# Kernel tuning notes

Measured on AMD Instinct MI355X. Metric: run time of the kernel, lower is better.

Reference implementation:

```python
import jax, jax.numpy as jnp
import numpy as np
from jax import lax

N_EXPERTS = 8


def setup_inputs() -> dict:
    key = jax.random.key(0)
    ks = jax.random.split(key, 5)
    B, F, H, C, E = 32768, 512, 256, 100, N_EXPERTS
    x = jax.random.normal(ks[0], (B, F), dtype=jnp.float32)
    W1 = jax.random.normal(ks[1], (E, F, H), dtype=jnp.float32) * (1.0 / np.sqrt(F))
    b1 = jnp.zeros((E, H), dtype=jnp.float32)
    W2 = jax.random.normal(ks[2], (E, H, C), dtype=jnp.float32) * (1.0 / np.sqrt(H))
    b2 = jnp.zeros((E, C), dtype=jnp.float32)
    Wg = jax.random.normal(ks[3], (F, E), dtype=jnp.float32) * (1.0 / np.sqrt(F))
    return {"x": x, "W1": W1, "b1": b1, "W2": W2, "b2": b2, "Wg": Wg, "k": 2}


def reference(x, W1, b1, W2, b2, Wg, k):
    B = x.shape[0]
    # experts: per-expert 2-layer MLP, vectorized over the expert dim e
    h = jax.nn.relu(jnp.einsum('bf,efh->ebh', x, W1) + b1[:, None, :])  # [E,B,H]
    preds = jnp.einsum('ebh,ehc->ebc', h, W2) + b2[:, None, :]          # [E,B,C]
    # fixed gating: softmax over gate logits, top-k, hard 1/k weights
    probs = jax.nn.softmax(x @ Wg, axis=-1)                             # [B,E]
    _, top_idx = lax.top_k(probs, k)                                    # [B,k]
    weights = jnp.zeros_like(probs).at[jnp.arange(B)[:, None], top_idx].set(1.0 / k)
    # combined prediction: gate-weighted sum of per-expert softmaxed logits
    combined = jnp.einsum('ebc,be->bc', jax.nn.softmax(preds, axis=-1), weights)
    part_sizes = (weights > 0).sum(axis=0)  # samples routed per expert
    return combined, preds, part_sizes
```

## Files before the change

kernel.cpp:

```cpp
#include <hip/hip_runtime.h>
#include <hip/hip_bf16.h>
#include <math.h>

#define B_ 32768
#define F_ 512
#define H_ 256
#define C_ 100
#define CP 112
#define E_ 8

typedef __attribute__((ext_vector_type(8))) short bf16x8;
typedef __attribute__((ext_vector_type(4))) float f32x4;

__device__ __forceinline__ unsigned short f2b(float f) {
    unsigned int u = __float_as_uint(f);
    return (unsigned short)((u + 0x7fffu + ((u >> 16) & 1u)) >> 16);
}

__device__ __forceinline__ void gll16(const void* g, void* l) {
    __builtin_amdgcn_global_load_lds((__attribute__((address_space(1))) void*)(g),
                                     (__attribute__((address_space(3))) void*)(l),
                                     16, 0, 0);
}

__global__ __launch_bounds__(256) void k0_cvt_x(const float* __restrict__ x,
                                                unsigned short* __restrict__ xb) {
    size_t t = (size_t)blockIdx.x * 256 + threadIdx.x;
    #pragma unroll
    for (int it = 0; it < 4; ++it) {
        size_t i4 = t + (size_t)it * (4096 * 256);
        float4 v = ((const float4*)x)[i4];
        ushort4 o;
        o.x = f2b(v.x); o.y = f2b(v.y); o.z = f2b(v.z); o.w = f2b(v.w);
        ((ushort4*)xb)[i4] = o;
    }
}

__global__ __launch_bounds__(256) void k0_tr_w1(const float* __restrict__ W1,
                                                unsigned short* __restrict__ w1t) {
    __shared__ float tile[32][33];
    int e = blockIdx.z, fb = blockIdx.x * 32, hb = blockIdx.y * 32;
    int tx = threadIdx.x, ty = threadIdx.y;
    #pragma unroll
    for (int j = 0; j < 4; ++j)
        tile[ty + 8 * j][tx] = W1[((size_t)(e * F_ + fb + ty + 8 * j)) * H_ + hb + tx];
    __syncthreads();
    #pragma unroll
    for (int j = 0; j < 4; ++j)
        w1t[((size_t)(e * H_ + hb + ty + 8 * j)) * F_ + fb + tx] = f2b(tile[tx][ty + 8 * j]);
}

__global__ __launch_bounds__(256) void k0_cvt_w2(const float* __restrict__ W2,
                                                 unsigned short* __restrict__ w2t) {
    int idx = blockIdx.x * 256 + threadIdx.x;
    if (idx >= E_ * CP * H_) return;
    int e = idx / (CP * H_);
    int r = idx - e * (CP * H_);
    int c = r / H_, h = r - c * H_;
    float v = (c < C_) ? W2[((size_t)(e * H_ + h)) * C_ + c] : 0.0f;
    w2t[idx] = f2b(v);
}

__global__ __launch_bounds__(256) void k1_gate(const float* __restrict__ x,
                                               const float* __restrict__ Wg,
                                               int* __restrict__ routes,
                                               float* __restrict__ part) {
    __shared__ float sWg[F_ * E_];
    __shared__ int cnt[E_];
    int tid = threadIdx.x;
    for (int i = tid; i < F_ * E_; i += 256) sWg[i] = Wg[i];
    if (tid < E_) cnt[tid] = 0;
    __syncthreads();

    int r = tid >> 3, eidx = tid & 7;
    int row = blockIdx.x * 32 + r;
    const float* xr = x + (size_t)row * F_;
    double acc = 0.0;
    for (int f = 0; f < F_; f += 4) {
        float4 xv = *(const float4*)(xr + f);
        acc += (double)xv.x * (double)sWg[(f + 0) * 8 + eidx];
        acc += (double)xv.y * (double)sWg[(f + 1) * 8 + eidx];
        acc += (double)xv.z * (double)sWg[(f + 2) * 8 + eidx];
        acc += (double)xv.w * (double)sWg[(f + 3) * 8 + eidx];
    }
    double v = acc; int ie = eidx;
    #pragma unroll
    for (int off = 1; off < 8; off <<= 1) {
        double ov = __shfl_xor(v, off);
        int oi = __shfl_xor(ie, off);
        if (ov > v || (ov == v && oi < ie)) { v = ov; ie = oi; }
    }
    int e1 = ie;
    double v2 = (eidx == e1) ? -1e300 : acc; int ie2 = eidx;
    #pragma unroll
    for (int off = 1; off < 8; off <<= 1) {
        double ov = __shfl_xor(v2, off);
        int oi = __shfl_xor(ie2, off);
        if (ov > v2 || (ov == v2 && oi < ie2)) { v2 = ov; ie2 = oi; }
    }
    int e2 = ie2;
    if (eidx == 0) {
        routes[row] = e1 | (e2 << 3);
        atomicAdd(&cnt[e1], 1);
        atomicAdd(&cnt[e2], 1);
    }
    __syncthreads();
    if (tid < E_) atomicAdd(&part[tid], (float)cnt[tid]);
}

__global__ __launch_bounds__(256) void k2_moe(const unsigned short* __restrict__ xbf,
                                              const unsigned short* __restrict__ w1t,
                                              const unsigned short* __restrict__ w2t,
                                              const float* __restrict__ b1,
                                              const float* __restrict__ b2,
                                              float* __restrict__ preds) {
    __shared__ __align__(16) char smem[40960];
    const int tid = threadIdx.x;
    const int w = tid >> 6, lane = tid & 63;
    const int q = lane >> 4, ln = lane & 15;
    const int e = blockIdx.y;
    const int rowBase = blockIdx.x * 64;

    const int sub = lane >> 3;
    const int j8 = (lane & 7) ^ sub;
    const unsigned short* srcA0 = xbf + (size_t)(rowBase + w * 8 + sub) * F_ + 8 * j8;
    const unsigned short* srcB0 = w1t + (size_t)(e * H_ + w * 8 + sub) * F_ + 8 * j8;
    char* dstA = smem + w * 1024;
    char* dstB = smem + 8192 + w * 1024;

    float bias1[4];
    #pragma unroll
    for (int nt = 0; nt < 4; ++nt) bias1[nt] = b1[e * H_ + w * 64 + nt * 16 + ln];

    f32x4 acc[4][4];
    #pragma unroll
    for (int i = 0; i < 4; ++i)
        #pragma unroll
        for (int j = 0; j < 4; ++j) acc[i][j] = (f32x4){0.f, 0.f, 0.f, 0.f};

    for (int kk = 0; kk < 8; ++kk) {
        const int ko = kk * 64;
        gll16(srcA0 + ko, dstA);
        gll16(srcA0 + 32 * F_ + ko, dstA + 4096);
        #pragma unroll
        for (int i = 0; i < 8; ++i)
            gll16(srcB0 + (size_t)i * 32 * F_ + ko, dstB + i * 4096);
        __syncthreads();
        #pragma unroll
        for (int ks = 0; ks < 2; ++ks) {
            const int slot = ((ks * 4 + q) ^ (ln & 7)) * 16;
            bf16x8 af[4], bfr[4];
            #pragma unroll
            for (int mt = 0; mt < 4; ++mt)
                af[mt] = *(const bf16x8*)(smem + (mt * 16 + ln) * 128 + slot);
            #pragma unroll
            for (int nt = 0; nt < 4; ++nt)
                bfr[nt] = *(const bf16x8*)(smem + 8192 + (w * 64 + nt * 16 + ln) * 128 + slot);
            #pragma unroll
            for (int mt = 0; mt < 4; ++mt)
                #pragma unroll
                for (int nt = 0; nt < 4; ++nt)
                    acc[mt][nt] = __builtin_amdgcn_mfma_f32_16x16x32_bf16(af[mt], bfr[nt], acc[mt][nt], 0, 0, 0);
        }
        __syncthreads();
    }

    #pragma unroll
    for (int mt = 0; mt < 4; ++mt)
        #pragma unroll
        for (int nt = 0; nt < 4; ++nt)
            #pragma unroll
            for (int r2 = 0; r2 < 4; ++r2) {
                int rr = mt * 16 + q * 4 + r2;
                int col = w * 64 + nt * 16 + ln;
                float v = fmaxf(acc[mt][nt][r2] + bias1[nt], 0.0f);
                *(unsigned short*)(smem + rr * 528 + col * 2) = f2b(v);
            }

    const unsigned short* w2base = w2t + ((size_t)e * CP + ln) * H_ + q * 8;
    bf16x8 wreg[2][7];
    #pragma unroll
    for (int mt = 0; mt < 7; ++mt)
        wreg[0][mt] = *(const bf16x8*)(w2base + mt * 16 * H_);

    f32x4 acc2[7];
    #pragma unroll
    for (int i = 0; i < 7; ++i) acc2[i] = (f32x4){0.f, 0.f, 0.f, 0.f};
    const int offH = (w * 16 + ln) * 528 + q * 16;

    __syncthreads();

    #pragma unroll
    for (int kc = 0; kc < 8; ++kc) {
        const int cur = kc & 1, nxt = cur ^ 1;
        if (kc < 7) {
            #pragma unroll
            for (int mt = 0; mt < 7; ++mt)
                wreg[nxt][mt] = *(const bf16x8*)(w2base + mt * 16 * H_ + (kc + 1) * 32);
        }
        bf16x8 hb = *(const bf16x8*)(smem + offH + kc * 64);
        #pragma unroll
        for (int mt = 0; mt < 7; ++mt)
            acc2[mt] = __builtin_amdgcn_mfma_f32_16x16x32_bf16(wreg[cur][mt], hb, acc2[mt], 0, 0, 0);
    }

    int row = rowBase + w * 16 + ln;
    #pragma unroll
    for (int mt = 0; mt < 7; ++mt) {
        int c0 = mt * 16 + q * 4;
        if (c0 + 3 < C_) {
            f32x4 bias = *(const f32x4*)(b2 + e * C_ + c0);
            f32x4 o = acc2[mt] + bias;
            *(f32x4*)(preds + ((size_t)e * B_ + row) * C_ + c0) = o;
        }
    }
}

__global__ __launch_bounds__(256) void k3_combine(const float* __restrict__ preds,
                                                  const int* __restrict__ routes,
                                                  float* __restrict__ combined) {
    __shared__ float pbuf[4][104];
    int tid = threadIdx.x, wv = tid >> 6, lane = tid & 63;
    int row = blockIdx.x * 2 + (wv >> 1);
    int rt = routes[row];
    int e = (wv & 1) ? ((rt >> 3) & 7) : (rt & 7);
    const float* pr = preds + ((size_t)e * B_ + row) * C_;
    float a0 = (lane < C_) ? pr[lane] : -1e30f;
    float a1 = (lane + 64 < C_) ? pr[lane + 64] : -1e30f;
    float m = fmaxf(a0, a1);
    #pragma unroll
    for (int off = 32; off; off >>= 1) m = fmaxf(m, __shfl_xor(m, off));
    float s0 = (lane < C_) ? expf(a0 - m) : 0.f;
    float s1 = (lane + 64 < C_) ? expf(a1 - m) : 0.f;
    float s = s0 + s1;
    #pragma unroll
    for (int off = 32; off; off >>= 1) s += __shfl_xor(s, off);
    float inv = 0.5f / s;
    if (lane < C_) pbuf[wv][lane] = s0 * inv;
    if (lane + 64 < C_) pbuf[wv][lane + 64] = s1 * inv;
    __syncthreads();
    if (tid < C_)
        combined[(size_t)(blockIdx.x * 2) * C_ + tid] = pbuf[0][tid] + pbuf[1][tid];
    else if (tid >= 128 && tid < 128 + C_)
        combined[(size_t)(blockIdx.x * 2 + 1) * C_ + (tid - 128)] = pbuf[2][tid - 128] + pbuf[3][tid - 128];
}

extern "C" void kernel_launch(void* const* d_in, const int* in_sizes, int n_in,
                              void* d_out, int out_size, void* d_ws, size_t ws_size,
                              hipStream_t stream) {
    (void)in_sizes; (void)n_in; (void)out_size;
    const float* x  = (const float*)d_in[0];
    const float* W1 = (const float*)d_in[1];
    const float* b1 = (const float*)d_in[2];
    const float* W2 = (const float*)d_in[3];
    const float* b2 = (const float*)d_in[4];
    const float* Wg = (const float*)d_in[5];

    float* out = (float*)d_out;
    float* combined = out;
    float* preds = out + (size_t)B_ * C_;
    float* part  = out + (size_t)B_ * C_ + (size_t)E_ * B_ * C_;

    char* ws = (char*)d_ws;
    unsigned short* xbf = (unsigned short*)ws;
    unsigned short* w1t = (unsigned short*)(ws + 33554432);
    unsigned short* w2t = (unsigned short*)(ws + 35651584);
    int* routes = (int*)(ws + 36110336);
    if (ws_size < 36241408) return;

    hipMemsetAsync(part, 0, E_ * sizeof(float), stream);
    k0_cvt_x<<<4096, 256, 0, stream>>>(x, xbf);
    k0_tr_w1<<<dim3(F_ / 32, H_ / 32, E_), dim3(32, 8), 0, stream>>>(W1, w1t);
    k0_cvt_w2<<<(E_ * CP * H_ + 255) / 256, 256, 0, stream>>>(W2, w2t);
    k1_gate<<<B_ / 32, 256, 0, stream>>>(x, Wg, routes, part);
    k2_moe<<<dim3(B_ / 64, E_), 256, 0, stream>>>(xbf, w1t, w2t, b1, b2, preds);
    k3_combine<<<B_ / 2, 256, 0, stream>>>(preds, routes, combined);
}
```

Baseline: 404.9 us.

## Fuse x bf16 conversion into gate kernel; stream W1 from global into registers

The separate x-to-bf16 conversion kernel is removed and its work moved into the gating kernel, which already reads x, so x is read from memory once instead of twice. In the MoE kernel the whole 64x512 A tile is loaded into LDS once (64KB) and the per-k-step syncthreads are gone. W1 fragments are now loaded straight from global memory into registers with one-step double buffering instead of being staged through LDS. This cuts barriers and LDS traffic. The cost is a larger LDS footprint, which limits occupancy to two blocks per CU, and W1 loads that depend on cache hits without coalescing through shared memory.

After: 460.5 us. 1.14x slower.

```diff
diff --git a/kernel.cpp b/kernel.cpp
--- a/kernel.cpp
+++ b/kernel.cpp
@@ -21,19 +21,6 @@
     __builtin_amdgcn_global_load_lds((__attribute__((address_space(1))) void*)(g),
                                      (__attribute__((address_space(3))) void*)(l),
                                      16, 0, 0);
-}
-
-__global__ __launch_bounds__(256) void k0_cvt_x(const float* __restrict__ x,
-                                                unsigned short* __restrict__ xb) {
-    size_t t = (size_t)blockIdx.x * 256 + threadIdx.x;
-    #pragma unroll
-    for (int it = 0; it < 4; ++it) {
-        size_t i4 = t + (size_t)it * (4096 * 256);
-        float4 v = ((const float4*)x)[i4];
-        ushort4 o;
-        o.x = f2b(v.x); o.y = f2b(v.y); o.z = f2b(v.z); o.w = f2b(v.w);
-        ((ushort4*)xb)[i4] = o;
-    }
 }
 
 __global__ __launch_bounds__(256) void k0_tr_w1(const float* __restrict__ W1,
@@ -63,6 +50,7 @@
 
 __global__ __launch_bounds__(256) void k1_gate(const float* __restrict__ x,
                                                const float* __restrict__ Wg,
+                                               unsigned short* __restrict__ xb,
                                                int* __restrict__ routes,
                                                float* __restrict__ part) {
     __shared__ float sWg[F_ * E_];
@@ -106,15 +94,25 @@
     }
     __syncthreads();
     if (tid < E_) atomicAdd(&part[tid], (float)cnt[tid]);
-}
-
-__global__ __launch_bounds__(256) void k2_moe(const unsigned short* __restrict__ xbf,
-                                              const unsigned short* __restrict__ w1t,
-                                              const unsigned short* __restrict__ w2t,
-                                              const float* __restrict__ b1,
-                                              const float* __restrict__ b2,
-                                              float* __restrict__ preds) {
-    __shared__ __align__(16) char smem[40960];
+
+    const float4* xs = (const float4*)(x + (size_t)blockIdx.x * 32 * F_);
+    ushort4* xd = (ushort4*)(xb + (size_t)blockIdx.x * 32 * F_);
+    #pragma unroll
+    for (int i = 0; i < 16; ++i) {
+        float4 xv = xs[tid + i * 256];
+        ushort4 o;
+        o.x = f2b(xv.x); o.y = f2b(xv.y); o.z = f2b(xv.z); o.w = f2b(xv.w);
+        xd[tid + i * 256] = o;
+    }
+}
+
+__global__ __launch_bounds__(256, 2) void k2_moe(const unsigned short* __restrict__ xbf,
+                                                 const unsigned short* __restrict__ w1t,
+                                                 const unsigned short* __restrict__ w2t,
+                                                 const float* __restrict__ b1,
+                                                 const float* __restrict__ b2,
+                                                 float* __restrict__ preds) {
+    __shared__ __align__(16) char smem[65536];
     const int tid = threadIdx.x;
     const int w = tid >> 6, lane = tid & 63;
     const int q = lane >> 4, ln = lane & 15;
@@ -124,9 +122,12 @@
     const int sub = lane >> 3;
     const int j8 = (lane & 7) ^ sub;
     const unsigned short* srcA0 = xbf + (size_t)(rowBase + w * 8 + sub) * F_ + 8 * j8;
-    const unsigned short* srcB0 = w1t + (size_t)(e * H_ + w * 8 + sub) * F_ + 8 * j8;
     char* dstA = smem + w * 1024;
-    char* dstB = smem + 8192 + w * 1024;
+    #pragma unroll
+    for (int kk = 0; kk < 8; ++kk) {
+        gll16(srcA0 + kk * 64, dstA + kk * 8192);
+        gll16(srcA0 + 32 * F_ + kk * 64, dstA + kk * 8192 + 4096);
+    }
 
     float bias1[4];
     #pragma unroll
@@ -138,32 +139,43 @@
         #pragma unroll
         for (int j = 0; j < 4; ++j) acc[i][j] = (f32x4){0.f, 0.f, 0.f, 0.f};
 
-    for (int kk = 0; kk < 8; ++kk) {
-        const int ko = kk * 64;
-        gll16(srcA0 + ko, dstA);
-        gll16(srcA0 + 32 * F_ + ko, dstA + 4096);
-        #pragma unroll
-        for (int i = 0; i < 8; ++i)
-            gll16(srcB0 + (size_t)i * 32 * F_ + ko, dstB + i * 4096);
-        __syncthreads();
-        #pragma unroll
-        for (int ks = 0; ks < 2; ++ks) {
-            const int slot = ((ks * 4 + q) ^ (ln & 7)) * 16;
-            bf16x8 af[4], bfr[4];
-            #pragma unroll
-            for (int mt = 0; mt < 4; ++mt)
-                af[mt] = *(const bf16x8*)(smem + (mt * 16 + ln) * 128 + slot);
+    const unsigned short* bb = w1t + ((size_t)e * H_ + w * 64 + ln) * F_ + q * 8;
+    bf16x8 bcur[4], bnxt[4];
+    #pragma unroll
+    for (int nt = 0; nt < 4; ++nt) bcur[nt] = *(const bf16x8*)(bb + nt * 16 * F_);
+
+    __syncthreads();
+
+    #pragma unroll
+    for (int h = 0; h < 16; ++h) {
+        const int kk = h >> 1, ks = h & 1;
+        if (h < 15) {
+            const int off2 = ((h + 1) >> 1) * 64 + ((h + 1) & 1) * 32;
             #pragma unroll
             for (int nt = 0; nt < 4; ++nt)
-                bfr[nt] = *(const bf16x8*)(smem + 8192 + (w * 64 + nt * 16 + ln) * 128 + slot);
-            #pragma unroll
-            for (int mt = 0; mt < 4; ++mt)
-                #pragma unroll
-                for (int nt = 0; nt < 4; ++nt)
-                    acc[mt][nt] = __builtin_amdgcn_mfma_f32_16x16x32_bf16(af[mt], bfr[nt], acc[mt][nt], 0, 0, 0);
+                bnxt[nt] = *(const bf16x8*)(bb + nt * 16 * F_ + off2);
         }
-        __syncthreads();
-    }
+        const int slot = ((ks * 4 + q) ^ (ln & 7)) * 16;
+        bf16x8 af[4];
+        #pragma unroll
+        for (int mt = 0; mt < 4; ++mt)
+            af[mt] = *(const bf16x8*)(smem + kk * 8192 + (mt * 16 + ln) * 128 + slot);
+        #pragma unroll
+        for (int mt = 0; mt < 4; ++mt)
+            #pragma unroll
+            for (int nt = 0; nt < 4; ++nt)
+                acc[mt][nt] = __builtin_amdgcn_mfma_f32_16x16x32_bf16(af[mt], bcur[nt], acc[mt][nt], 0, 0, 0);
+        #pragma unroll
+        for (int nt = 0; nt < 4; ++nt) bcur[nt] = bnxt[nt];
+    }
+
+    __syncthreads();
+
+    const unsigned short* w2base = w2t + ((size_t)e * CP + ln) * H_ + q * 8;
+    bf16x8 wreg[2][7];
+    #pragma unroll
+    for (int mt = 0; mt < 7; ++mt)
+        wreg[0][mt] = *(const bf16x8*)(w2base + mt * 16 * H_);
 
     #pragma unroll
     for (int mt = 0; mt < 4; ++mt)
@@ -176,12 +188,6 @@
                 float v = fmaxf(acc[mt][nt][r2] + bias1[nt], 0.0f);
                 *(unsigned short*)(smem + rr * 528 + col * 2) = f2b(v);
             }
-
-    const unsigned short* w2base = w2t + ((size_t)e * CP + ln) * H_ + q * 8;
-    bf16x8 wreg[2][7];
-    #pragma unroll
-    for (int mt = 0; mt < 7; ++mt)
-        wreg[0][mt] = *(const bf16x8*)(w2base + mt * 16 * H_);
 
     f32x4 acc2[7];
     #pragma unroll
@@ -269,10 +275,9 @@
     if (ws_size < 36241408) return;
 
     hipMemsetAsync(part, 0, E_ * sizeof(float), stream);
-    k0_cvt_x<<<4096, 256, 0, stream>>>(x, xbf);
     k0_tr_w1<<<dim3(F_ / 32, H_ / 32, E_), dim3(32, 8), 0, stream>>>(W1, w1t);
     k0_cvt_w2<<<(E_ * CP * H_ + 255) / 256, 256, 0, stream>>>(W2, w2t);
-    k1_gate<<<B_ / 32, 256, 0, stream>>>(x, Wg, routes, part);
+    k1_gate<<<B_ / 32, 256, 0, stream>>>(x, Wg, xbf, routes, part);
     k2_moe<<<dim3(B_ / 64, E_), 256, 0, stream>>>(xbf, w1t, w2t, b1, b2, preds);
     k3_combine<<<B_ / 2, 256, 0, stream>>>(preds, routes, combined);
 }
```
